# Kernel optimization log

Measured on AMD Instinct MI355X. Metric: run time of the kernel, lower is better.

## Reference

```python
import jax, jax.numpy as jnp
import numpy as np

D = 768       # feature dim (LayerNorm([768]))
NCHAR = 96    # codebook rows (char_dic = zeros(96, 768))
EPS = 1e-5    # torch LayerNorm default eps
EMA = 0.1     # EMA update coefficient


def layer_norm(x, w, b):
    mu = jnp.mean(x, axis=-1, keepdims=True)
    var = jnp.mean((x - mu) ** 2, axis=-1, keepdims=True)
    return (x - mu) * jax.lax.rsqrt(var + EPS) * w + b


def setup_inputs() -> dict:
    key = jax.random.key(0)
    k1, k2, k3 = jax.random.split(key, 3)
    B, S = 128, 1024
    return {
        "input_f": jax.random.normal(k1, (B, S, D), dtype=jnp.float32),
        "char_dic": jax.random.normal(k2, (NCHAR, D), dtype=jnp.float32),
        "ln_w": jnp.ones((D,), dtype=jnp.float32),
        "ln_b": jnp.zeros((D,), dtype=jnp.float32),
        "target": jax.random.randint(k3, (B, S), 0, NCHAR),
    }


def reference(input_f, char_dic, ln_w, ln_b, target):
    x = layer_norm(input_f, ln_w, ln_b)              # [B, S, D]
    flat = x.reshape(-1, D)                          # [N, D]
    labels = target.reshape(-1)                      # [N]
    # per-label scatter-add of token embeddings
    tok_sums = jax.ops.segment_sum(flat, labels, num_segments=NCHAR)          # [96, D]
    counts = jax.ops.segment_sum(jnp.ones_like(labels, dtype=jnp.float32),
                                 labels, num_segments=NCHAR)                  # [96]
    # group i = [char_dic[i]] + tokens with label i; row-sum of that group:
    group_sum = char_dic + tok_sums
    # sum of all pairwise dot products within a group == ||row-sum||^2
    positive = jnp.sum(group_sum * group_sum) / D
    # EMA codebook update (rows 1..95 only; row 0 untouched)
    mean = group_sum / (counts + 1.0)[:, None]       # group size = n_i + 1 (dic row)
    upd = char_dic + EMA * mean
    new_char = jnp.where(jnp.arange(NCHAR)[:, None] >= 1, upd, char_dic)
    # torch applies layer_norm1 to the updated codebook under no_grad
    normed = jax.lax.stop_gradient(layer_norm(new_char, ln_w, ln_b))
    s = jnp.sum(normed[1:], axis=0)                  # sum-of-rows identity again
    negative = jnp.dot(s, s) / D
    return negative - positive
```

## Files before the change

### kernel.cpp

```cpp
#include <hip/hip_runtime.h>

#define DD 768
#define NCH 96
#define NBLK 128
#define SUBCAP 64
#define NSLOT (NCH * NBLK)
#define MGRID (NSLOT / 4)

__device__ __forceinline__ float wave_reduce_sum(float v) {
#pragma unroll
  for (int m = 32; m >= 1; m >>= 1) v += __shfl_xor(v, m, 64);
  return v;
}

__global__ void __launch_bounds__(256) k_scatter(const int* __restrict__ tgt, int n, int chunk,
                                                 int* __restrict__ sorted, int* __restrict__ pcnt,
                                                 float* __restrict__ gS, float* __restrict__ gpos,
                                                 int* __restrict__ ctr) {
  __shared__ int lh[NCH];
  int tid = threadIdx.x, bid = blockIdx.x;
  if (tid < NCH) lh[tid] = 0;
  if (bid == 0) {
    for (int i = tid; i < DD; i += 256) gS[i] = 0.f;
    if (tid == 0) { gpos[0] = 0.f; ctr[0] = 0; }
  }
  __syncthreads();
  int beg = bid * chunk, end = min(beg + chunk, n);
  for (int i = beg + tid; i < end; i += 256) {
    int c = tgt[i];
    int r = atomicAdd(&lh[c], 1);
    if (r < SUBCAP) sorted[(size_t)(c * NBLK + bid) * SUBCAP + r] = i;
  }
  __syncthreads();
  if (tid < NCH) pcnt[tid * NBLK + bid] = min(lh[tid], SUBCAP);
}

__device__ __forceinline__ void load_row(const float* __restrict__ x, int t, int lane,
                                         float4& A, float4& B, float4& C) {
  const float4* r = (const float4*)(x + (size_t)t * DD);
  A = r[lane]; B = r[64 + lane]; C = r[128 + lane];
}

__device__ __forceinline__ void red_row(const float4& A, const float4& B, const float4& C,
                                        float acc[12], float& mcp) {
  float v[12] = {A.x, A.y, A.z, A.w, B.x, B.y, B.z, B.w, C.x, C.y, C.z, C.w};
  float s = 0.f, q = 0.f;
#pragma unroll
  for (int k = 0; k < 12; ++k) { s += v[k]; q += v[k] * v[k]; }
  s = wave_reduce_sum(s);
  q = wave_reduce_sum(q);
  float mu = s * (1.f / DD);
  float rstd = rsqrtf(q * (1.f / DD) - mu * mu + 1e-5f);
#pragma unroll
  for (int k = 0; k < 12; ++k) acc[k] += rstd * v[k];
  mcp += rstd * mu;
}

__global__ void __launch_bounds__(256) k_main(
    const float* __restrict__ x, const int* __restrict__ sorted,
    const int* __restrict__ pcnt,
    float* __restrict__ P, float* __restrict__ Pm) {
  int lane = threadIdx.x & 63;
  int s = (blockIdx.x * blockDim.x + threadIdx.x) >> 6;
  if (s >= NSLOT) return;
  int cnt = pcnt[s];
  if (cnt == 0) return;

  int tl = (lane < cnt) ? sorted[(size_t)s * SUBCAP + lane] : 0;
  float acc[12];
#pragma unroll
  for (int k = 0; k < 12; ++k) acc[k] = 0.f;
  float mcp = 0.f;

  float4 A0, B0, C0, A1, B1, C1;
  load_row(x, __shfl(tl, 0), lane, A0, B0, C0);
  if (cnt > 1) load_row(x, __shfl(tl, 1), lane, A1, B1, C1);
  for (int i = 0; i < cnt; ++i) {
    float4 A2, B2, C2;
    if (i + 2 < cnt) load_row(x, __shfl(tl, i + 2), lane, A2, B2, C2);
    red_row(A0, B0, C0, acc, mcp);
    A0 = A1; B0 = B1; C0 = C1;
    A1 = A2; B1 = B2; C1 = C2;
  }

  float4* Pr = (float4*)(P + (size_t)s * DD);
  Pr[lane]       = make_float4(acc[0], acc[1], acc[2], acc[3]);
  Pr[64 + lane]  = make_float4(acc[4], acc[5], acc[6], acc[7]);
  Pr[128 + lane] = make_float4(acc[8], acc[9], acc[10], acc[11]);
  if (lane == 0) Pm[s] = mcp;
}

__global__ void __launch_bounds__(256) k_finish(
    const float* __restrict__ dic, const float* __restrict__ wv_,
    const float* __restrict__ bv_, const float* __restrict__ P,
    const float* __restrict__ Pm, const int* __restrict__ pcnt,
    float* __restrict__ gS, float* __restrict__ gpos, int* __restrict__ counter,
    float* __restrict__ out) {
  __shared__ float accsh[DD];
  __shared__ float mcsh, ncsh;
  int c = blockIdx.x, tid = threadIdx.x, lane = tid & 63, wid = tid >> 6;
  for (int i = tid; i < DD; i += 256) accsh[i] = 0.f;
  if (tid == 0) { mcsh = 0.f; ncsh = 0.f; }
  __syncthreads();

  float acc[12];
#pragma unroll
  for (int k = 0; k < 12; ++k) acc[k] = 0.f;
  float mcp = 0.f, ncp = 0.f;
  for (int j = wid; j < NBLK; j += 4) {
    int s = c * NBLK + j;
    int cnt = pcnt[s];
    if (cnt == 0) continue;
    ncp += (float)cnt;
    const float4* Pr = (const float4*)(P + (size_t)s * DD);
    float4 A = Pr[lane], B = Pr[64 + lane], C = Pr[128 + lane];
    acc[0] += A.x; acc[1] += A.y; acc[2]  += A.z; acc[3]  += A.w;
    acc[4] += B.x; acc[5] += B.y; acc[6]  += B.z; acc[7]  += B.w;
    acc[8] += C.x; acc[9] += C.y; acc[10] += C.z; acc[11] += C.w;
    mcp += Pm[s];
  }
#pragma unroll
  for (int k = 0; k < 12; ++k) {
    int d = (k >> 2) * 256 + 4 * lane + (k & 3);
    atomicAdd(&accsh[d], acc[k]);
  }
  if (lane == 0) { atomicAdd(&mcsh, mcp); atomicAdd(&ncsh, ncp); }
  __syncthreads();

  if (wid == 0) {
    float mc = mcsh;
    float nc = ncsh;
    float g[12], pacc = 0.f;
#pragma unroll
    for (int k = 0; k < 12; ++k) {
      int d = (k >> 2) * 256 + 4 * lane + (k & 3);
      float gg = dic[c * DD + d] + wv_[d] * (accsh[d] - mc) + nc * bv_[d];
      g[k] = gg; pacc += gg * gg;
    }
    pacc = wave_reduce_sum(pacc);
    if (lane == 0) atomicAdd(gpos, pacc);
    if (c >= 1) {
      float inv = 1.f / (nc + 1.f);
      float u[12], sum = 0.f, sq = 0.f;
#pragma unroll
      for (int k = 0; k < 12; ++k) {
        int d = (k >> 2) * 256 + 4 * lane + (k & 3);
        float uu = dic[c * DD + d] + 0.1f * g[k] * inv;
        u[k] = uu; sum += uu; sq += uu * uu;
      }
      sum = wave_reduce_sum(sum);
      sq = wave_reduce_sum(sq);
      float mu = sum * (1.f / DD);
      float rstd = rsqrtf(sq * (1.f / DD) - mu * mu + 1e-5f);
#pragma unroll
      for (int k = 0; k < 12; ++k) {
        int d = (k >> 2) * 256 + 4 * lane + (k & 3);
        atomicAdd(&gS[d], (u[k] - mu) * rstd * wv_[d] + bv_[d]);
      }
    }
    __threadfence();
    int done = 0;
    if (lane == 0) done = (atomicAdd(counter, 1) == NCH - 1) ? 1 : 0;
    done = __shfl(done, 0);
    if (done) {
      __threadfence();
      float nv = 0.f;
#pragma unroll
      for (int k = 0; k < 12; ++k) {
        int d = (k >> 2) * 256 + 4 * lane + (k & 3);
        float t = gS[d];
        nv += t * t;
      }
      nv = wave_reduce_sum(nv);
      if (lane == 0) out[0] = (nv - gpos[0]) * (1.f / DD);
    }
  }
}

extern "C" void kernel_launch(void* const* d_in, const int* in_sizes, int n_in,
                              void* d_out, int out_size, void* d_ws, size_t ws_size,
                              hipStream_t stream) {
  (void)n_in; (void)out_size; (void)ws_size;
  const float* x   = (const float*)d_in[0];
  const float* dic = (const float*)d_in[1];
  const float* w   = (const float*)d_in[2];
  const float* b   = (const float*)d_in[3];
  const int*   tgt = (const int*)d_in[4];
  float* out = (float*)d_out;
  int N = in_sizes[4];

  char* ws = (char*)d_ws;
  float* gS     = (float*)(ws);
  float* gpos   = (float*)(ws + 3072);
  int*   ctr    = (int*)(ws + 3076);
  int*   pcnt   = (int*)(ws + 4096);
  float* Pm     = (float*)(ws + 4096 + NSLOT * 4);
  size_t o_sorted = 4096 + (size_t)NSLOT * 8;
  int*   sorted = (int*)(ws + o_sorted);
  size_t o_P = (o_sorted + (size_t)NSLOT * SUBCAP * 4 + 255) & ~(size_t)255;
  float* P = (float*)(ws + o_P);

  int chunk = (N + NBLK - 1) / NBLK;
  k_scatter<<<NBLK, 256, 0, stream>>>(tgt, N, chunk, sorted, pcnt, gS, gpos, ctr);
  k_main<<<MGRID, 256, 0, stream>>>(x, sorted, pcnt, P, Pm);
  k_finish<<<NCH, 256, 0, stream>>>(dic, w, b, P, Pm, pcnt, gS, gpos, ctr, out);
}
```

Measured before the change: 135.8 us.

## Store per-slot partial sums as bf16 and widen finish kernel to 1024 threads

Per-slot partial LayerNorm sums are packed to bf16 pairs, which halves the intermediate write and read traffic between the main and finish kernels. The main kernel now reads token indices through scalar loads (readfirstlane) instead of a lane-wide load plus shuffles, and always issues prefetch loads with a clamped index. The finish kernel uses 16 waves per codebook row and computes counts separately. The bf16 rounding of partial sums adds precision loss to the final scalar.

```diff
diff --git a/kernel.cpp b/kernel.cpp
--- a/kernel.cpp
+++ b/kernel.cpp
@@ -12,6 +12,16 @@
   for (int m = 32; m >= 1; m >>= 1) v += __shfl_xor(v, m, 64);
   return v;
 }
+
+__device__ __forceinline__ unsigned int bf2(float a, float b) {
+  unsigned int ua = __float_as_uint(a);
+  ua += 0x7fffu + ((ua >> 16) & 1u);
+  unsigned int ub = __float_as_uint(b);
+  ub += 0x7fffu + ((ub >> 16) & 1u);
+  return (ua >> 16) | (ub & 0xffff0000u);
+}
+__device__ __forceinline__ float bflo(unsigned int u) { return __uint_as_float(u << 16); }
+__device__ __forceinline__ float bfhi(unsigned int u) { return __uint_as_float(u & 0xffff0000u); }
 
 __global__ void __launch_bounds__(256) k_scatter(const int* __restrict__ tgt, int n, int chunk,
                                                  int* __restrict__ sorted, int* __restrict__ pcnt,
@@ -59,72 +69,75 @@
 __global__ void __launch_bounds__(256) k_main(
     const float* __restrict__ x, const int* __restrict__ sorted,
     const int* __restrict__ pcnt,
-    float* __restrict__ P, float* __restrict__ Pm) {
+    unsigned int* __restrict__ P16, float* __restrict__ Pm) {
   int lane = threadIdx.x & 63;
   int s = (blockIdx.x * blockDim.x + threadIdx.x) >> 6;
-  if (s >= NSLOT) return;
+  s = __builtin_amdgcn_readfirstlane(s);
   int cnt = pcnt[s];
   if (cnt == 0) return;
-
-  int tl = (lane < cnt) ? sorted[(size_t)s * SUBCAP + lane] : 0;
+  const int* lst = sorted + (size_t)s * SUBCAP;
+
   float acc[12];
 #pragma unroll
   for (int k = 0; k < 12; ++k) acc[k] = 0.f;
   float mcp = 0.f;
 
+  int t0 = lst[0];
+  int t1 = lst[cnt > 1 ? 1 : 0];
   float4 A0, B0, C0, A1, B1, C1;
-  load_row(x, __shfl(tl, 0), lane, A0, B0, C0);
-  if (cnt > 1) load_row(x, __shfl(tl, 1), lane, A1, B1, C1);
+  load_row(x, t0, lane, A0, B0, C0);
+  load_row(x, t1, lane, A1, B1, C1);
   for (int i = 0; i < cnt; ++i) {
+    int tn = lst[(i + 2 < cnt) ? (i + 2) : (cnt - 1)];
     float4 A2, B2, C2;
-    if (i + 2 < cnt) load_row(x, __shfl(tl, i + 2), lane, A2, B2, C2);
+    load_row(x, tn, lane, A2, B2, C2);
     red_row(A0, B0, C0, acc, mcp);
     A0 = A1; B0 = B1; C0 = C1;
     A1 = A2; B1 = B2; C1 = C2;
   }
 
-  float4* Pr = (float4*)(P + (size_t)s * DD);
-  Pr[lane]       = make_float4(acc[0], acc[1], acc[2], acc[3]);
-  Pr[64 + lane]  = make_float4(acc[4], acc[5], acc[6], acc[7]);
-  Pr[128 + lane] = make_float4(acc[8], acc[9], acc[10], acc[11]);
+  unsigned int* Pr = P16 + (size_t)s * (DD / 2);
+#pragma unroll
+  for (int m = 0; m < 6; ++m) Pr[m * 64 + lane] = bf2(acc[2 * m], acc[2 * m + 1]);
   if (lane == 0) Pm[s] = mcp;
 }
 
-__global__ void __launch_bounds__(256) k_finish(
+__global__ void __launch_bounds__(1024) k_finish(
     const float* __restrict__ dic, const float* __restrict__ wv_,
-    const float* __restrict__ bv_, const float* __restrict__ P,
+    const float* __restrict__ bv_, const unsigned int* __restrict__ P16,
     const float* __restrict__ Pm, const int* __restrict__ pcnt,
     float* __restrict__ gS, float* __restrict__ gpos, int* __restrict__ counter,
     float* __restrict__ out) {
   __shared__ float accsh[DD];
   __shared__ float mcsh, ncsh;
   int c = blockIdx.x, tid = threadIdx.x, lane = tid & 63, wid = tid >> 6;
-  for (int i = tid; i < DD; i += 256) accsh[i] = 0.f;
+  if (tid < DD) accsh[tid] = 0.f;
   if (tid == 0) { mcsh = 0.f; ncsh = 0.f; }
   __syncthreads();
 
   float acc[12];
 #pragma unroll
   for (int k = 0; k < 12; ++k) acc[k] = 0.f;
-  float mcp = 0.f, ncp = 0.f;
-  for (int j = wid; j < NBLK; j += 4) {
-    int s = c * NBLK + j;
-    int cnt = pcnt[s];
-    if (cnt == 0) continue;
-    ncp += (float)cnt;
-    const float4* Pr = (const float4*)(P + (size_t)s * DD);
-    float4 A = Pr[lane], B = Pr[64 + lane], C = Pr[128 + lane];
-    acc[0] += A.x; acc[1] += A.y; acc[2]  += A.z; acc[3]  += A.w;
-    acc[4] += B.x; acc[5] += B.y; acc[6]  += B.z; acc[7]  += B.w;
-    acc[8] += C.x; acc[9] += C.y; acc[10] += C.z; acc[11] += C.w;
-    mcp += Pm[s];
+  float mcp = 0.f;
+  for (int j = wid; j < NBLK; j += 16) {
+    int sl = c * NBLK + j;
+    if (pcnt[sl] == 0) continue;
+    const unsigned int* Pr = P16 + (size_t)sl * (DD / 2);
+#pragma unroll
+    for (int m = 0; m < 6; ++m) {
+      unsigned int u = Pr[m * 64 + lane];
+      acc[2 * m]     += bflo(u);
+      acc[2 * m + 1] += bfhi(u);
+    }
+    mcp += Pm[sl];
   }
 #pragma unroll
   for (int k = 0; k < 12; ++k) {
     int d = (k >> 2) * 256 + 4 * lane + (k & 3);
     atomicAdd(&accsh[d], acc[k]);
   }
-  if (lane == 0) { atomicAdd(&mcsh, mcp); atomicAdd(&ncsh, ncp); }
+  if (lane == 0) atomicAdd(&mcsh, mcp);
+  if (tid < NBLK) atomicAdd(&ncsh, (float)pcnt[c * NBLK + tid]);
   __syncthreads();
 
   if (wid == 0) {
@@ -195,13 +208,12 @@
   int*   ctr    = (int*)(ws + 3076);
   int*   pcnt   = (int*)(ws + 4096);
   float* Pm     = (float*)(ws + 4096 + NSLOT * 4);
-  size_t o_sorted = 4096 + (size_t)NSLOT * 8;
+  unsigned int* P16 = (unsigned int*)(ws + 102400);
+  size_t o_sorted = 102400 + (size_t)NSLOT * (DD / 2) * 4;
   int*   sorted = (int*)(ws + o_sorted);
-  size_t o_P = (o_sorted + (size_t)NSLOT * SUBCAP * 4 + 255) & ~(size_t)255;
-  float* P = (float*)(ws + o_P);
 
   int chunk = (N + NBLK - 1) / NBLK;
   k_scatter<<<NBLK, 256, 0, stream>>>(tgt, N, chunk, sorted, pcnt, gS, gpos, ctr);
-  k_main<<<MGRID, 256, 0, stream>>>(x, sorted, pcnt, P, Pm);
-  k_finish<<<NCH, 256, 0, stream>>>(dic, w, b, P, Pm, pcnt, gS, gpos, ctr, out);
-}
+  k_main<<<MGRID, 256, 0, stream>>>(x, sorted, pcnt, P16, Pm);
+  k_finish<<<NCH, 1024, 0, stream>>>(dic, w, b, P16, Pm, pcnt, gS, gpos, ctr, out);
+}
```

Result: no change. 133.3 us (-1.9%).
